# Optimization experiments

Measured on AMD Instinct MI355X. Metric: run time of the kernel, lower is better.

Reference implementation:

```python
import jax, jax.numpy as jnp
import numpy as np

B, N, K = 4, 32768, 16
IN_DIM, HID, OUT_DIM = 32, 64, 32
N_DIM = 2
KIN = 2 * N_DIM + OUT_DIM  # 36
KH = 64
EPS = 1e-5


def _gelu(x):
    return jax.nn.gelu(x, approximate=False)  # torch F.gelu default (erf)


def setup_inputs() -> dict:
    key = jax.random.key(0)
    ks = jax.random.split(key, 16)
    s = lambda fan_in: 1.0 / np.sqrt(fan_in)
    return {
        "inp": jax.random.normal(ks[0], (B, N, IN_DIM), jnp.float32),
        "input_grid": jax.random.uniform(ks[1], (N, N_DIM), jnp.float32),
        "output_grid": jax.random.uniform(ks[2], (N, N_DIM), jnp.float32),
        "neighbor_idx": jax.random.randint(ks[3], (N, K), 0, N, jnp.int32),
        # pointwise projection MLP: in_dim -> hid -> out_dim, GELU between
        "Wp1": jax.random.normal(ks[4], (IN_DIM, HID), jnp.float32) * s(IN_DIM),
        "bp1": jnp.zeros((HID,), jnp.float32),
        "Wp2": jax.random.normal(ks[5], (HID, OUT_DIM), jnp.float32) * s(HID),
        "bp2": jnp.zeros((OUT_DIM,), jnp.float32),
        # per-edge kernel MLP: [2*n_dim+out_dim, 64, 64, out_dim], GELU between
        "Wk1": jax.random.normal(ks[6], (KIN, KH), jnp.float32) * s(KIN),
        "bk1": jnp.zeros((KH,), jnp.float32),
        "Wk2": jax.random.normal(ks[7], (KH, KH), jnp.float32) * s(KH),
        "bk2": jnp.zeros((KH,), jnp.float32),
        "Wk3": jax.random.normal(ks[8], (KH, OUT_DIM), jnp.float32) * s(KH),
        "bk3": jnp.zeros((OUT_DIM,), jnp.float32),
        # LayerNorm
        "ln_gamma": jnp.ones((OUT_DIM,), jnp.float32),
        "ln_beta": jnp.zeros((OUT_DIM,), jnp.float32),
    }


def reference(inp, input_grid, output_grid, neighbor_idx,
              Wp1, bp1, Wp2, bp2, Wk1, bk1, Wk2, bk2, Wk3, bk3,
              ln_gamma, ln_beta):
    # pointwise projection MLP
    x = _gelu(jnp.einsum('bnc,ch->bnh', inp, Wp1) + bp1)
    x = jnp.einsum('bnh,ho->bno', x, Wp2) + bp2  # (B, N, OUT_DIM)

    # neighbor gather (fixed K neighbors per output point)
    f_y = x[:, neighbor_idx, :]                      # (B, N, K, C)
    y_pos = input_grid[neighbor_idx]                 # (N, K, n_dim)
    x_pos = jnp.broadcast_to(output_grid[:, None, :], (N, K, N_DIM))
    pos_feat = jnp.concatenate([y_pos, x_pos], axis=-1)          # (N, K, 2*n_dim)
    agg = jnp.concatenate(
        [jnp.broadcast_to(pos_feat[None], (x.shape[0], N, K, 2 * N_DIM)), f_y],
        axis=-1)                                      # (B, N, K, KIN)

    # nonlinear kernel MLP k(x, y, f(y))
    h = _gelu(jnp.einsum('bnkc,ch->bnkh', agg, Wk1) + bk1)
    h = _gelu(jnp.einsum('bnkh,hg->bnkg', h, Wk2) + bk2)
    k_out = jnp.einsum('bnkg,go->bnko', h, Wk3) + bk3  # (B, N, K, OUT_DIM)

    # mean-aggregate over neighbors (integral transform)
    out = jnp.mean(k_out, axis=2)                      # (B, N, OUT_DIM)

    # residual (shapes match) + LayerNorm over channels
    out = out + x
    mu = jnp.mean(out, axis=-1, keepdims=True)
    var = jnp.mean((out - mu) ** 2, axis=-1, keepdims=True)
    out = (out - mu) * jax.lax.rsqrt(var + EPS) * ln_gamma + ln_beta
    return out
```

## Files before the change

### kernel.cpp

```cpp
#include <hip/hip_runtime.h>

#define BB 4
#define NN 32768
#define KKN 16
#define IN_DIM 32
#define HID 64
#define OUT_DIM 32
#define KH 64
#define WS 88
#define TOT (BB * NN)
#define NWAVES 4096

typedef _Float16 f16;
typedef f16 f16x2 __attribute__((ext_vector_type(2)));
typedef f16 f16x4 __attribute__((ext_vector_type(4)));
typedef f16 f16x8 __attribute__((ext_vector_type(8)));
typedef float f32x4 __attribute__((ext_vector_type(4)));
typedef __fp16 hf16x2 __attribute__((ext_vector_type(2)));

#define H2(c) ((f16x2){(f16)(c), (f16)(c)})

__device__ __forceinline__ f16x2 cvt2(float a, float b) {
    hf16x2 r = __builtin_amdgcn_cvt_pkrtz(a, b);
    return __builtin_bit_cast(f16x2, r);
}

__device__ __forceinline__ f16x2 gelu2(float a, float b) {
    f16x2 x  = cvt2(a, b);
    f16x2 s  = __builtin_elementwise_min(
                   __builtin_elementwise_max(x, H2(-3.5f)), H2(3.5f));
    f16x2 s4 = s * H2(0.25f);
    f16x2 t  = s4 * s4;
    f16x2 g  = H2(-1.0110344f);
    g = g * t + H2( 2.85016064f);
    g = g * t + H2(-3.40439040f);
    g = g * t + H2( 2.32402432f);
    g = g * t + H2(-1.04974080f);
    g = g * t + H2( 0.39879504f);
    f16x2 f  = s * g;
    f16x2 hx = x * H2(0.5f);
    return x * f + hx;
}

template <int CTRL>
__device__ __forceinline__ float dppadd(float v) {
    union { float f; int i; } u, r;
    u.f = v;
    r.i = __builtin_amdgcn_update_dpp(0, u.i, CTRL, 0xf, 0xf, true);
    return v + r.f;
}
__device__ __forceinline__ float rowsum16(float v) {
    v = dppadd<0xB1>(v);
    v = dppadd<0x4E>(v);
    v = dppadd<0x124>(v);
    v = dppadd<0x128>(v);
    return v;
}

__global__ __launch_bounds__(256) void point_mlp_kernel(
    const float* __restrict__ inp, const float* __restrict__ Wp1,
    const float* __restrict__ bp1, const float* __restrict__ Wp2,
    const float* __restrict__ bp2, f16* __restrict__ xhf)
{
    __shared__ __align__(16) f16 hb[4][16 * WS];
    const int tid = threadIdx.x, w = tid >> 6, lane = tid & 63;
    const int q = lane >> 4, nl = lane & 15;

    f16x8 w1f[4];
    #pragma unroll
    for (int nb = 0; nb < 4; nb++)
        #pragma unroll
        for (int j = 0; j < 8; j++)
            w1f[nb][j] = (f16)Wp1[(q * 8 + j) * HID + nb * 16 + nl];
    f16x8 w2f[2][2];
    #pragma unroll
    for (int nb = 0; nb < 2; nb++)
        #pragma unroll
        for (int c = 0; c < 2; c++)
            #pragma unroll
            for (int j = 0; j < 8; j++) {
                int k = c * 32 + q * 8 + j, kp = ((k & 3) << 4) | (k >> 2);
                w2f[nb][c][j] = (f16)Wp2[kp * OUT_DIM + nb * 16 + nl];
            }
    float b1v[4], b2v[2];
    #pragma unroll
    for (int nb = 0; nb < 4; nb++) b1v[nb] = bp1[nb * 16 + nl];
    b2v[0] = bp2[nl]; b2v[1] = bp2[16 + nl];

    const int gw = blockIdx.x * 4 + w;
    const int nw = gridDim.x * 4;

    for (int t = gw; t < TOT / 16; t += nw) {
        const int R = t * 16;
        const float* ap = inp + (size_t)(R + nl) * IN_DIM + q * 8;
        float4 av0 = *(const float4*)ap, av1 = *(const float4*)(ap + 4);
        f16x2 p01 = cvt2(av0.x, av0.y);
        f16x2 p23 = cvt2(av0.z, av0.w);
        f16x2 p45 = cvt2(av1.x, av1.y);
        f16x2 p67 = cvt2(av1.z, av1.w);
        f16x8 af = (f16x8){p01.x, p01.y, p23.x, p23.y, p45.x, p45.y, p67.x, p67.y};

        f32x4 acc[4];
        #pragma unroll
        for (int nb = 0; nb < 4; nb++)
            acc[nb] = (f32x4){b1v[nb], b1v[nb], b1v[nb], b1v[nb]};
        #pragma unroll
        for (int nb = 0; nb < 4; nb++)
            acc[nb] = __builtin_amdgcn_mfma_f32_16x16x32_f16(af, w1f[nb], acc[nb], 0, 0, 0);

        #pragma unroll
        for (int r = 0; r < 4; r++) {
            f16x2 h01 = gelu2(acc[0][r], acc[1][r]);
            f16x2 h23 = gelu2(acc[2][r], acc[3][r]);
            *(f16x4*)&hb[w][(q * 4 + r) * WS + nl * 4] = (f16x4){h01.x, h01.y, h23.x, h23.y};
        }
        f16x8 a0 = *(const f16x8*)&hb[w][nl * WS + q * 8];
        f16x8 a1 = *(const f16x8*)&hb[w][nl * WS + 32 + q * 8];
        f32x4 a2[2];
        #pragma unroll
        for (int nb = 0; nb < 2; nb++) {
            a2[nb] = (f32x4){b2v[nb], b2v[nb], b2v[nb], b2v[nb]};
            a2[nb] = __builtin_amdgcn_mfma_f32_16x16x32_f16(a0, w2f[nb][0], a2[nb], 0, 0, 0);
            a2[nb] = __builtin_amdgcn_mfma_f32_16x16x32_f16(a1, w2f[nb][1], a2[nb], 0, 0, 0);
        }
        #pragma unroll
        for (int r = 0; r < 4; r++)
            #pragma unroll
            for (int nb = 0; nb < 2; nb++)
                xhf[(size_t)(R + q * 4 + r) * OUT_DIM + nb * 16 + nl] = (f16)a2[nb][r];
    }
}

__global__ __launch_bounds__(256) void gnn_edge_kernel(
    const f16*   __restrict__ xhf,
    const float* __restrict__ igrid, const float* __restrict__ ogrid,
    const int*   __restrict__ nbi,
    const float* __restrict__ Wk1, const float* __restrict__ bk1,
    const float* __restrict__ Wk2, const float* __restrict__ bk2,
    const float* __restrict__ Wk3, const float* __restrict__ bk3,
    const float* __restrict__ gma, const float* __restrict__ bta,
    float* __restrict__ out)
{
    __shared__ __align__(16) f16 tile[8][16 * WS];

    const int tid = threadIdx.x, w = tid >> 6, lane = tid & 63;
    const int q = lane >> 4, nl = lane & 15;
    f16* __restrict__ TA = tile[w * 2];
    f16* __restrict__ TB = tile[w * 2 + 1];

    f16x8 w1f[4][2], w2f[4][2], w3f[2][2];
    #pragma unroll
    for (int nb = 0; nb < 4; nb++) {
        #pragma unroll
        for (int j = 0; j < 8; j++) {
            w1f[nb][0][j] = (f16)Wk1[(4 + q * 8 + j) * KH + nb * 16 + nl];
            float v1 = 0.0f;
            if (j < 4 && q == 0) v1 = Wk1[j * KH + nb * 16 + nl];
            w1f[nb][1][j] = (f16)v1;
        }
        #pragma unroll
        for (int c = 0; c < 2; c++)
            #pragma unroll
            for (int j = 0; j < 8; j++) {
                int k = c * 32 + q * 8 + j, kp = ((k & 3) << 4) | (k >> 2);
                w2f[nb][c][j] = (f16)Wk2[kp * KH + nb * 16 + nl];
            }
    }
    #pragma unroll
    for (int nb = 0; nb < 2; nb++)
        #pragma unroll
        for (int c = 0; c < 2; c++)
            #pragma unroll
            for (int j = 0; j < 8; j++) {
                int k = c * 32 + q * 8 + j, kp = ((k & 3) << 4) | (k >> 2);
                w3f[nb][c][j] = (f16)Wk3[kp * OUT_DIM + nb * 16 + nl];
            }

    float b1v[4], b2v[4], b3v[2];
    #pragma unroll
    for (int nb = 0; nb < 4; nb++) { b1v[nb] = bk1[nb * 16 + nl]; b2v[nb] = bk2[nb * 16 + nl]; }
    b3v[0] = bk3[nl]; b3v[1] = bk3[16 + nl];
    const float g0 = gma[nl], g1 = gma[16 + nl], be0 = bta[nl], be1 = bta[16 + nl];

    const int gw = blockIdx.x * 4 + w;
    const int e = lane >> 2, part = lane & 3;

    {
        const f16x8 zf = {(f16)0.f,(f16)0.f,(f16)0.f,(f16)0.f,(f16)0.f,(f16)0.f,(f16)0.f,(f16)0.f};
        for (int i = lane * 8; i < 16 * WS; i += 64 * 8) { *(f16x8*)&TA[i] = zf; *(f16x8*)&TB[i] = zf; }
    }

    int tA = gw, tB = gw + NWAVES;
    int nA = nbi[(tA & (NN - 1)) * KKN + e];
    int nB = nbi[(tB & (NN - 1)) * KKN + e];
    uint4 fyA = ((const uint4*)(xhf + ((size_t)((tA >> 15) * NN + nA)) * OUT_DIM))[part];
    uint4 fyB = ((const uint4*)(xhf + ((size_t)((tB >> 15) * NN + nB)) * OUT_DIM))[part];
    float2 ipA, opA, ipB, opB;
    if (part == 0) {
        ipA = ((const float2*)igrid)[nA]; opA = ((const float2*)ogrid)[tA & (NN - 1)];
        ipB = ((const float2*)igrid)[nB]; opB = ((const float2*)ogrid)[tB & (NN - 1)];
    }
    f16 xA0 = xhf[(size_t)tA * OUT_DIM + nl],      xA1 = xhf[(size_t)tA * OUT_DIM + 16 + nl];
    f16 xB0 = xhf[(size_t)tB * OUT_DIM + nl],      xB1 = xhf[(size_t)tB * OUT_DIM + 16 + nl];

    #pragma unroll 1
    for (int it = 0; it < TOT / (2 * NWAVES); ++it) {
        *(uint4*)&TA[e * WS + part * 8] = fyA;
        *(uint4*)&TB[e * WS + part * 8] = fyB;
        if (part == 0) {
            f16x4 pA = {(f16)ipA.x, (f16)ipA.y, (f16)opA.x, (f16)opA.y};
            f16x4 pB = {(f16)ipB.x, (f16)ipB.y, (f16)opB.x, (f16)opB.y};
            *(f16x4*)&TA[e * WS + 32] = pA;
            *(f16x4*)&TB[e * WS + 32] = pB;
        }
        const float rA0 = (float)xA0, rA1 = (float)xA1, rB0 = (float)xB0, rB1 = (float)xB1;

        const int tA2 = (tA + 2 * NWAVES) & (TOT - 1);
        const int tB2 = tA2 + NWAVES;
        const int nA2 = nbi[(tA2 & (NN - 1)) * KKN + e];
        const int nB2 = nbi[(tB2 & (NN - 1)) * KKN + e];

        f16x8 aA0 = *(const f16x8*)&TA[nl * WS + q * 8];
        f16x8 aA1 = *(const f16x8*)&TA[nl * WS + 32 + q * 8];
        f16x8 aB0 = *(const f16x8*)&TB[nl * WS + q * 8];
        f16x8 aB1 = *(const f16x8*)&TB[nl * WS + 32 + q * 8];
        f32x4 cA[4], cB[4];
        #pragma unroll
        for (int nb = 0; nb < 4; nb++) {
            cA[nb] = (f32x4){b1v[nb], b1v[nb], b1v[nb], b1v[nb]};
            cB[nb] = (f32x4){b1v[nb], b1v[nb], b1v[nb], b1v[nb]};
        }
        #pragma unroll
        for (int nb = 0; nb < 4; nb++) {
            cA[nb] = __builtin_amdgcn_mfma_f32_16x16x32_f16(aA0, w1f[nb][0], cA[nb], 0, 0, 0);
            cB[nb] = __builtin_amdgcn_mfma_f32_16x16x32_f16(aB0, w1f[nb][0], cB[nb], 0, 0, 0);
            cA[nb] = __builtin_amdgcn_mfma_f32_16x16x32_f16(aA1, w1f[nb][1], cA[nb], 0, 0, 0);
            cB[nb] = __builtin_amdgcn_mfma_f32_16x16x32_f16(aB1, w1f[nb][1], cB[nb], 0, 0, 0);
        }
        #pragma unroll
        for (int r = 0; r < 4; r++) {
            f16x2 hA01 = gelu2(cA[0][r], cA[1][r]);
            f16x2 hA23 = gelu2(cA[2][r], cA[3][r]);
            f16x2 hB01 = gelu2(cB[0][r], cB[1][r]);
            f16x2 hB23 = gelu2(cB[2][r], cB[3][r]);
            *(f16x4*)&TA[(q * 4 + r) * WS + nl * 4] = (f16x4){hA01.x, hA01.y, hA23.x, hA23.y};
            *(f16x4*)&TB[(q * 4 + r) * WS + nl * 4] = (f16x4){hB01.x, hB01.y, hB23.x, hB23.y};
        }

        uint4 fyA2 = ((const uint4*)(xhf + ((size_t)((tA2 >> 15) * NN + nA2)) * OUT_DIM))[part];
        uint4 fyB2 = ((const uint4*)(xhf + ((size_t)((tB2 >> 15) * NN + nB2)) * OUT_DIM))[part];
        float2 ipA2, opA2, ipB2, opB2;
        if (part == 0) {
            ipA2 = ((const float2*)igrid)[nA2]; opA2 = ((const float2*)ogrid)[tA2 & (NN - 1)];
            ipB2 = ((const float2*)igrid)[nB2]; opB2 = ((const float2*)ogrid)[tB2 & (NN - 1)];
        }
        f16 xA0n = xhf[(size_t)tA2 * OUT_DIM + nl],  xA1n = xhf[(size_t)tA2 * OUT_DIM + 16 + nl];
        f16 xB0n = xhf[(size_t)tB2 * OUT_DIM + nl],  xB1n = xhf[(size_t)tB2 * OUT_DIM + 16 + nl];

        aA0 = *(const f16x8*)&TA[nl * WS + q * 8];
        aA1 = *(const f16x8*)&TA[nl * WS + 32 + q * 8];
        aB0 = *(const f16x8*)&TB[nl * WS + q * 8];
        aB1 = *(const f16x8*)&TB[nl * WS + 32 + q * 8];
        #pragma unroll
        for (int nb = 0; nb < 4; nb++) {
            cA[nb] = (f32x4){b2v[nb], b2v[nb], b2v[nb], b2v[nb]};
            cB[nb] = (f32x4){b2v[nb], b2v[nb], b2v[nb], b2v[nb]};
        }
        #pragma unroll
        for (int nb = 0; nb < 4; nb++) {
            cA[nb] = __builtin_amdgcn_mfma_f32_16x16x32_f16(aA0, w2f[nb][0], cA[nb], 0, 0, 0);
            cB[nb] = __builtin_amdgcn_mfma_f32_16x16x32_f16(aB0, w2f[nb][0], cB[nb], 0, 0, 0);
            cA[nb] = __builtin_amdgcn_mfma_f32_16x16x32_f16(aA1, w2f[nb][1], cA[nb], 0, 0, 0);
            cB[nb] = __builtin_amdgcn_mfma_f32_16x16x32_f16(aB1, w2f[nb][1], cB[nb], 0, 0, 0);
        }
        #pragma unroll
        for (int r = 0; r < 4; r++) {
            f16x2 hA01 = gelu2(cA[0][r], cA[1][r]);
            f16x2 hA23 = gelu2(cA[2][r], cA[3][r]);
            f16x2 hB01 = gelu2(cB[0][r], cB[1][r]);
            f16x2 hB23 = gelu2(cB[2][r], cB[3][r]);
            *(f16x4*)&TA[(q * 4 + r) * WS + nl * 4] = (f16x4){hA01.x, hA01.y, hA23.x, hA23.y};
            *(f16x4*)&TB[(q * 4 + r) * WS + nl * 4] = (f16x4){hB01.x, hB01.y, hB23.x, hB23.y};
        }

        aA0 = *(const f16x8*)&TA[nl * WS + q * 8];
        aA1 = *(const f16x8*)&TA[nl * WS + 32 + q * 8];
        aB0 = *(const f16x8*)&TB[nl * WS + q * 8];
        aB1 = *(const f16x8*)&TB[nl * WS + 32 + q * 8];
        f32x4 dA[2], dB[2];
        #pragma unroll
        for (int nb = 0; nb < 2; nb++) {
            dA[nb] = (f32x4){0.f, 0.f, 0.f, 0.f};
            dB[nb] = (f32x4){0.f, 0.f, 0.f, 0.f};
            dA[nb] = __builtin_amdgcn_mfma_f32_16x16x32_f16(aA0, w3f[nb][0], dA[nb], 0, 0, 0);
            dB[nb] = __builtin_amdgcn_mfma_f32_16x16x32_f16(aB0, w3f[nb][0], dB[nb], 0, 0, 0);
            dA[nb] = __builtin_amdgcn_mfma_f32_16x16x32_f16(aA1, w3f[nb][1], dA[nb], 0, 0, 0);
            dB[nb] = __builtin_amdgcn_mfma_f32_16x16x32_f16(aB1, w3f[nb][1], dB[nb], 0, 0, 0);
        }

        {
            float s0 = dA[0][0] + dA[0][1] + dA[0][2] + dA[0][3];
            float s1 = dA[1][0] + dA[1][1] + dA[1][2] + dA[1][3];
            float u0 = dB[0][0] + dB[0][1] + dB[0][2] + dB[0][3];
            float u1 = dB[1][0] + dB[1][1] + dB[1][2] + dB[1][3];
            s0 += __shfl_xor(s0, 16, 64); s0 += __shfl_xor(s0, 32, 64);
            s1 += __shfl_xor(s1, 16, 64); s1 += __shfl_xor(s1, 32, 64);
            u0 += __shfl_xor(u0, 16, 64); u0 += __shfl_xor(u0, 32, 64);
            u1 += __shfl_xor(u1, 16, 64); u1 += __shfl_xor(u1, 32, 64);

            float oA0 = s0 * 0.0625f + b3v[0] + rA0;
            float oA1 = s1 * 0.0625f + b3v[1] + rA1;
            float oB0 = u0 * 0.0625f + b3v[0] + rB0;
            float oB1 = u1 * 0.0625f + b3v[1] + rB1;

            float mA = rowsum16(oA0 + oA1) * (1.0f / 32.0f);
            float mB = rowsum16(oB0 + oB1) * (1.0f / 32.0f);
            float dA0 = oA0 - mA, dA1 = oA1 - mA, dB0 = oB0 - mB, dB1 = oB1 - mB;
            float vA = rowsum16(dA0 * dA0 + dA1 * dA1) * (1.0f / 32.0f);
            float vB = rowsum16(dB0 * dB0 + dB1 * dB1) * (1.0f / 32.0f);
            float rsA = rsqrtf(vA + 1e-5f);
            float rsB = rsqrtf(vB + 1e-5f);

            if (q == 0) {
                float* oa = out + (size_t)tA * OUT_DIM;
                float* ob = out + (size_t)tB * OUT_DIM;
                oa[nl]      = fmaf(dA0 * rsA, g0, be0);
                oa[16 + nl] = fmaf(dA1 * rsA, g1, be1);
                ob[nl]      = fmaf(dB0 * rsB, g0, be0);
                ob[16 + nl] = fmaf(dB1 * rsB, g1, be1);
            }
        }

        tA = tA2; tB = tB2;
        fyA = fyA2; fyB = fyB2;
        ipA = ipA2; opA = opA2; ipB = ipB2; opB = opB2;
        xA0 = xA0n; xA1 = xA1n; xB0 = xB0n; xB1 = xB1n;
    }
}

extern "C" void kernel_launch(void* const* d_in, const int* in_sizes, int n_in,
                              void* d_out, int out_size, void* d_ws, size_t ws_size,
                              hipStream_t stream) {
    const float* inp   = (const float*)d_in[0];
    const float* igrid = (const float*)d_in[1];
    const float* ogrid = (const float*)d_in[2];
    const int*   nbi   = (const int*)d_in[3];
    const float* Wp1   = (const float*)d_in[4];
    const float* bp1   = (const float*)d_in[5];
    const float* Wp2   = (const float*)d_in[6];
    const float* bp2   = (const float*)d_in[7];
    const float* Wk1   = (const float*)d_in[8];
    const float* bk1   = (const float*)d_in[9];
    const float* Wk2   = (const float*)d_in[10];
    const float* bk2   = (const float*)d_in[11];
    const float* Wk3   = (const float*)d_in[12];
    const float* bk3   = (const float*)d_in[13];
    const float* gma   = (const float*)d_in[14];
    const float* bta   = (const float*)d_in[15];
    float* out = (float*)d_out;
    f16* xhf = (f16*)d_ws;

    point_mlp_kernel<<<1024, 256, 0, stream>>>(inp, Wp1, bp1, Wp2, bp2, xhf);
    gnn_edge_kernel<<<1024, 256, 0, stream>>>(xhf, igrid, ogrid, nbi,
                                              Wk1, bk1, Wk2, bk2, Wk3, bk3,
                                              gma, bta, out);
}
```

Baseline: 206.0 us.

## Build first-layer MFMA operands via ds_bpermute instead of LDS staging

Replaces the LDS store-then-load staging of gathered neighbor features and position features for the first kernel MLP layer with cross-lane ds_bpermute shuffles straight into the MFMA A-operand registers. The upper K half is zero-filled in registers, which drops the LDS zero-initialisation. The GELU polynomial tail is simplified to one fewer multiply, and the point MLP launch grid is halved. Each operand word now costs its own bpermute, and halving the point-MLP grid changes that kernel's work per block and occupancy. If the point-MLP kernel's loop does not scale with the grid size, the half grid could leave part of the projection uncomputed.

```diff
diff --git a/kernel.cpp b/kernel.cpp
--- a/kernel.cpp
+++ b/kernel.cpp
@@ -17,6 +17,7 @@
 typedef f16 f16x8 __attribute__((ext_vector_type(8)));
 typedef float f32x4 __attribute__((ext_vector_type(4)));
 typedef __fp16 hf16x2 __attribute__((ext_vector_type(2)));
+typedef unsigned int u32x4 __attribute__((ext_vector_type(4)));
 
 #define H2(c) ((f16x2){(f16)(c), (f16)(c)})
 
@@ -37,9 +38,8 @@
     g = g * t + H2( 2.32402432f);
     g = g * t + H2(-1.04974080f);
     g = g * t + H2( 0.39879504f);
-    f16x2 f  = s * g;
-    f16x2 hx = x * H2(0.5f);
-    return x * f + hx;
+    f16x2 h  = s * g + H2(0.5f);
+    return x * h;
 }
 
 template <int CTRL>
@@ -184,35 +184,28 @@
 
     const int gw = blockIdx.x * 4 + w;
     const int e = lane >> 2, part = lane & 3;
-
-    {
-        const f16x8 zf = {(f16)0.f,(f16)0.f,(f16)0.f,(f16)0.f,(f16)0.f,(f16)0.f,(f16)0.f,(f16)0.f};
-        for (int i = lane * 8; i < 16 * WS; i += 64 * 8) { *(f16x8*)&TA[i] = zf; *(f16x8*)&TB[i] = zf; }
-    }
+    const int bp = (nl * 4 + q) * 4;
 
     int tA = gw, tB = gw + NWAVES;
     int nA = nbi[(tA & (NN - 1)) * KKN + e];
     int nB = nbi[(tB & (NN - 1)) * KKN + e];
     uint4 fyA = ((const uint4*)(xhf + ((size_t)((tA >> 15) * NN + nA)) * OUT_DIM))[part];
     uint4 fyB = ((const uint4*)(xhf + ((size_t)((tB >> 15) * NN + nB)) * OUT_DIM))[part];
-    float2 ipA, opA, ipB, opB;
+    uint2 paA, paB;
     if (part == 0) {
-        ipA = ((const float2*)igrid)[nA]; opA = ((const float2*)ogrid)[tA & (NN - 1)];
-        ipB = ((const float2*)igrid)[nB]; opB = ((const float2*)ogrid)[tB & (NN - 1)];
+        float2 ip, op;
+        ip = ((const float2*)igrid)[nA]; op = ((const float2*)ogrid)[tA & (NN - 1)];
+        paA.x = __builtin_bit_cast(unsigned, cvt2(ip.x, ip.y));
+        paA.y = __builtin_bit_cast(unsigned, cvt2(op.x, op.y));
+        ip = ((const float2*)igrid)[nB]; op = ((const float2*)ogrid)[tB & (NN - 1)];
+        paB.x = __builtin_bit_cast(unsigned, cvt2(ip.x, ip.y));
+        paB.y = __builtin_bit_cast(unsigned, cvt2(op.x, op.y));
     }
     f16 xA0 = xhf[(size_t)tA * OUT_DIM + nl],      xA1 = xhf[(size_t)tA * OUT_DIM + 16 + nl];
     f16 xB0 = xhf[(size_t)tB * OUT_DIM + nl],      xB1 = xhf[(size_t)tB * OUT_DIM + 16 + nl];
 
     #pragma unroll 1
     for (int it = 0; it < TOT / (2 * NWAVES); ++it) {
-        *(uint4*)&TA[e * WS + part * 8] = fyA;
-        *(uint4*)&TB[e * WS + part * 8] = fyB;
-        if (part == 0) {
-            f16x4 pA = {(f16)ipA.x, (f16)ipA.y, (f16)opA.x, (f16)opA.y};
-            f16x4 pB = {(f16)ipB.x, (f16)ipB.y, (f16)opB.x, (f16)opB.y};
-            *(f16x4*)&TA[e * WS + 32] = pA;
-            *(f16x4*)&TB[e * WS + 32] = pB;
-        }
         const float rA0 = (float)xA0, rA1 = (float)xA1, rB0 = (float)xB0, rB1 = (float)xB1;
 
         const int tA2 = (tA + 2 * NWAVES) & (TOT - 1);
@@ -220,10 +213,26 @@
         const int nA2 = nbi[(tA2 & (NN - 1)) * KKN + e];
         const int nB2 = nbi[(tB2 & (NN - 1)) * KKN + e];
 
-        f16x8 aA0 = *(const f16x8*)&TA[nl * WS + q * 8];
-        f16x8 aA1 = *(const f16x8*)&TA[nl * WS + 32 + q * 8];
-        f16x8 aB0 = *(const f16x8*)&TB[nl * WS + q * 8];
-        f16x8 aB1 = *(const f16x8*)&TB[nl * WS + 32 + q * 8];
+        u32x4 sA, sB;
+        sA.x = (unsigned)__builtin_amdgcn_ds_bpermute(bp, (int)fyA.x);
+        sA.y = (unsigned)__builtin_amdgcn_ds_bpermute(bp, (int)fyA.y);
+        sA.z = (unsigned)__builtin_amdgcn_ds_bpermute(bp, (int)fyA.z);
+        sA.w = (unsigned)__builtin_amdgcn_ds_bpermute(bp, (int)fyA.w);
+        sB.x = (unsigned)__builtin_amdgcn_ds_bpermute(bp, (int)fyB.x);
+        sB.y = (unsigned)__builtin_amdgcn_ds_bpermute(bp, (int)fyB.y);
+        sB.z = (unsigned)__builtin_amdgcn_ds_bpermute(bp, (int)fyB.z);
+        sB.w = (unsigned)__builtin_amdgcn_ds_bpermute(bp, (int)fyB.w);
+        f16x8 aA0 = __builtin_bit_cast(f16x8, sA);
+        f16x8 aB0 = __builtin_bit_cast(f16x8, sB);
+        unsigned pa0 = (unsigned)__builtin_amdgcn_ds_bpermute(bp, (int)paA.x);
+        unsigned pa1 = (unsigned)__builtin_amdgcn_ds_bpermute(bp, (int)paA.y);
+        unsigned pb0 = (unsigned)__builtin_amdgcn_ds_bpermute(bp, (int)paB.x);
+        unsigned pb1 = (unsigned)__builtin_amdgcn_ds_bpermute(bp, (int)paB.y);
+        u32x4 uA1 = (u32x4){q == 0 ? pa0 : 0u, q == 0 ? pa1 : 0u, 0u, 0u};
+        u32x4 uB1 = (u32x4){q == 0 ? pb0 : 0u, q == 0 ? pb1 : 0u, 0u, 0u};
+        f16x8 aA1 = __builtin_bit_cast(f16x8, uA1);
+        f16x8 aB1 = __builtin_bit_cast(f16x8, uB1);
+
         f32x4 cA[4], cB[4];
         #pragma unroll
         for (int nb = 0; nb < 4; nb++) {
@@ -249,18 +258,23 @@
 
         uint4 fyA2 = ((const uint4*)(xhf + ((size_t)((tA2 >> 15) * NN + nA2)) * OUT_DIM))[part];
         uint4 fyB2 = ((const uint4*)(xhf + ((size_t)((tB2 >> 15) * NN + nB2)) * OUT_DIM))[part];
-        float2 ipA2, opA2, ipB2, opB2;
+        uint2 paA2, paB2;
         if (part == 0) {
-            ipA2 = ((const float2*)igrid)[nA2]; opA2 = ((const float2*)ogrid)[tA2 & (NN - 1)];
-            ipB2 = ((const float2*)igrid)[nB2]; opB2 = ((const float2*)ogrid)[tB2 & (NN - 1)];
+            float2 ip, op;
+            ip = ((const float2*)igrid)[nA2]; op = ((const float2*)ogrid)[tA2 & (NN - 1)];
+            paA2.x = __builtin_bit_cast(unsigned, cvt2(ip.x, ip.y));
+            paA2.y = __builtin_bit_cast(unsigned, cvt2(op.x, op.y));
+            ip = ((const float2*)igrid)[nB2]; op = ((const float2*)ogrid)[tB2 & (NN - 1)];
+            paB2.x = __builtin_bit_cast(unsigned, cvt2(ip.x, ip.y));
+            paB2.y = __builtin_bit_cast(unsigned, cvt2(op.x, op.y));
         }
         f16 xA0n = xhf[(size_t)tA2 * OUT_DIM + nl],  xA1n = xhf[(size_t)tA2 * OUT_DIM + 16 + nl];
         f16 xB0n = xhf[(size_t)tB2 * OUT_DIM + nl],  xB1n = xhf[(size_t)tB2 * OUT_DIM + 16 + nl];
 
-        aA0 = *(const f16x8*)&TA[nl * WS + q * 8];
-        aA1 = *(const f16x8*)&TA[nl * WS + 32 + q * 8];
-        aB0 = *(const f16x8*)&TB[nl * WS + q * 8];
-        aB1 = *(const f16x8*)&TB[nl * WS + 32 + q * 8];
+        f16x8 bA0 = *(const f16x8*)&TA[nl * WS + q * 8];
+        f16x8 bA1 = *(const f16x8*)&TA[nl * WS + 32 + q * 8];
+        f16x8 bB0 = *(const f16x8*)&TB[nl * WS + q * 8];
+        f16x8 bB1 = *(const f16x8*)&TB[nl * WS + 32 + q * 8];
         #pragma unroll
         for (int nb = 0; nb < 4; nb++) {
             cA[nb] = (f32x4){b2v[nb], b2v[nb], b2v[nb], b2v[nb]};
@@ -268,10 +282,10 @@
         }
         #pragma unroll
         for (int nb = 0; nb < 4; nb++) {
-            cA[nb] = __builtin_amdgcn_mfma_f32_16x16x32_f16(aA0, w2f[nb][0], cA[nb], 0, 0, 0);
-            cB[nb] = __builtin_amdgcn_mfma_f32_16x16x32_f16(aB0, w2f[nb][0], cB[nb], 0, 0, 0);
-            cA[nb] = __builtin_amdgcn_mfma_f32_16x16x32_f16(aA1, w2f[nb][1], cA[nb], 0, 0, 0);
-            cB[nb] = __builtin_amdgcn_mfma_f32_16x16x32_f16(aB1, w2f[nb][1], cB[nb], 0, 0, 0);
+            cA[nb] = __builtin_amdgcn_mfma_f32_16x16x32_f16(bA0, w2f[nb][0], cA[nb], 0, 0, 0);
+            cB[nb] = __builtin_amdgcn_mfma_f32_16x16x32_f16(bB0, w2f[nb][0], cB[nb], 0, 0, 0);
+            cA[nb] = __builtin_amdgcn_mfma_f32_16x16x32_f16(bA1, w2f[nb][1], cA[nb], 0, 0, 0);
+            cB[nb] = __builtin_amdgcn_mfma_f32_16x16x32_f16(bB1, w2f[nb][1], cB[nb], 0, 0, 0);
         }
         #pragma unroll
         for (int r = 0; r < 4; r++) {
@@ -283,19 +297,19 @@
             *(f16x4*)&TB[(q * 4 + r) * WS + nl * 4] = (f16x4){hB01.x, hB01.y, hB23.x, hB23.y};
         }
 
-        aA0 = *(const f16x8*)&TA[nl * WS + q * 8];
-        aA1 = *(const f16x8*)&TA[nl * WS + 32 + q * 8];
-        aB0 = *(const f16x8*)&TB[nl * WS + q * 8];
-        aB1 = *(const f16x8*)&TB[nl * WS + 32 + q * 8];
+        bA0 = *(const f16x8*)&TA[nl * WS + q * 8];
+        bA1 = *(const f16x8*)&TA[nl * WS + 32 + q * 8];
+        bB0 = *(const f16x8*)&TB[nl * WS + q * 8];
+        bB1 = *(const f16x8*)&TB[nl * WS + 32 + q * 8];
         f32x4 dA[2], dB[2];
         #pragma unroll
         for (int nb = 0; nb < 2; nb++) {
             dA[nb] = (f32x4){0.f, 0.f, 0.f, 0.f};
             dB[nb] = (f32x4){0.f, 0.f, 0.f, 0.f};
-            dA[nb] = __builtin_amdgcn_mfma_f32_16x16x32_f16(aA0, w3f[nb][0], dA[nb], 0, 0, 0);
-            dB[nb] = __builtin_amdgcn_mfma_f32_16x16x32_f16(aB0, w3f[nb][0], dB[nb], 0, 0, 0);
-            dA[nb] = __builtin_amdgcn_mfma_f32_16x16x32_f16(aA1, w3f[nb][1], dA[nb], 0, 0, 0);
-            dB[nb] = __builtin_amdgcn_mfma_f32_16x16x32_f16(aB1, w3f[nb][1], dB[nb], 0, 0, 0);
+            dA[nb] = __builtin_amdgcn_mfma_f32_16x16x32_f16(bA0, w3f[nb][0], dA[nb], 0, 0, 0);
+            dB[nb] = __builtin_amdgcn_mfma_f32_16x16x32_f16(bB0, w3f[nb][0], dB[nb], 0, 0, 0);
+            dA[nb] = __builtin_amdgcn_mfma_f32_16x16x32_f16(bA1, w3f[nb][1], dA[nb], 0, 0, 0);
+            dB[nb] = __builtin_amdgcn_mfma_f32_16x16x32_f16(bB1, w3f[nb][1], dB[nb], 0, 0, 0);
         }
 
         {
@@ -333,7 +347,7 @@
 
         tA = tA2; tB = tB2;
         fyA = fyA2; fyB = fyB2;
-        ipA = ipA2; opA = opA2; ipB = ipB2; opB = opB2;
+        paA = paA2; paB = paB2;
         xA0 = xA0n; xA1 = xA1n; xB0 = xB0n; xB1 = xB1n;
     }
 }
@@ -360,7 +374,7 @@
     float* out = (float*)d_out;
     f16* xhf = (f16*)d_ws;
 
-    point_mlp_kernel<<<1024, 256, 0, stream>>>(inp, Wp1, bp1, Wp2, bp2, xhf);
+    point_mlp_kernel<<<512, 256, 0, stream>>>(inp, Wp1, bp1, Wp2, bp2, xhf);
     gnn_edge_kernel<<<1024, 256, 0, stream>>>(xhf, igrid, ogrid, nbi,
                                               Wk1, bk1, Wk2, bk2, Wk3, bk3,
                                               gma, bta, out);
```

Result: slower. 216.0 us (+4.9%).
